# Performance work log

Measured on AMD Instinct MI355X. Metric: run time of the kernel, lower is better.

Reference implementation:

```python
import jax, jax.numpy as jnp
import numpy as np
from jax import lax

# Module constants (from init_kwargs)
B, C = 2, 64            # batch, in_channel
H, W, D = 64, 64, 64    # size
GROUPS = 2


def setup_inputs() -> dict:
    key = jax.random.key(0)
    ks = jax.random.split(key, 4)
    x = jax.random.normal(ks[0], (B, H * W * D, C), dtype=jnp.float32)
    # TransverseConv: Conv3d(2, W*2, (H,3,3), pad (0,1,1)) -> weight (O,I,kD,kH,kW)
    w_t = jax.random.normal(ks[1], (W * GROUPS, GROUPS, H, 3, 3), dtype=jnp.float32) * 0.02
    b_t = jnp.zeros((W * GROUPS,), jnp.float32)
    # CoronalConv: Conv3d(2, W*2, (3,3,D), pad (1,1,0))
    w_c = jax.random.normal(ks[2], (W * GROUPS, GROUPS, 3, 3, D), dtype=jnp.float32) * 0.02
    b_c = jnp.zeros((W * GROUPS,), jnp.float32)
    # map: Conv3d(2C, C, 1) stored as dense (C, 2C)
    w_map = jax.random.normal(ks[3], (C, 2 * C), dtype=jnp.float32) * 0.02
    b_map = jnp.zeros((C,), jnp.float32)
    return {"x": x, "w_t": w_t, "b_t": b_t, "w_c": w_c, "b_c": b_c,
            "w_map": w_map, "b_map": b_map}


def _forward(x, w_t, b_t, w_c, b_c, w_map, b_map):
    Bx, N, Cx = x.shape
    xg = x.transpose(0, 2, 1).reshape(Bx, Cx, H, W, D)   # (B,C,H,W,D)
    shortcut = xg
    xr = xg.reshape(Bx * Cx // GROUPS, GROUPS, H, W, D)
    dn = ('NCDHW', 'OIDHW', 'NCDHW')
    # Transverse: kernel spans full H -> output (B*C/2, 2W, 1, W, D)
    tans = lax.conv_general_dilated(xr, w_t, (1, 1, 1), [(0, 0), (1, 1), (1, 1)],
                                    dimension_numbers=dn)
    tans = tans + b_t[None, :, None, None, None]
    tans = tans.reshape(Bx, Cx, W, W, D)                 # (B,C,W,W,D)
    # Coronal: kernel spans full D -> output (B*C/2, 2W, H, W, 1)
    cor = lax.conv_general_dilated(xr, w_c, (1, 1, 1), [(1, 1), (1, 1), (0, 0)],
                                   dimension_numbers=dn)
    cor = cor + b_c[None, :, None, None, None]
    cor = cor.reshape(Bx, Cx, W, H, W)                   # (B,C,W,H,W)
    t1 = tans.transpose(0, 1, 3, 2, 4)                   # (B,C,W,W,D)
    c1 = cor.transpose(0, 1, 4, 3, 2)                    # (B,C,W,H,W)
    f = jnp.matmul(c1, t1).transpose(0, 1, 3, 2, 4)      # (B,C,H,W,D)
    attn = jnp.matmul(cor, tans).transpose(0, 1, 3, 2, 4)  # (B,C,H,W,D)
    cat = jnp.concatenate([shortcut * f, attn], axis=1)  # (B,2C,H,W,D)
    mapped = jnp.einsum('bkhwd,ck->bchwd', cat, w_map) + b_map[None, :, None, None, None]
    out = jax.nn.gelu(mapped, approximate=False)         # torch nn.GELU = exact erf
    return out.reshape(Bx, Cx, -1).transpose(0, 2, 1)    # (B,N,C)


def reference(x, w_t, b_t, w_c, b_c, w_map, b_map):
    return _forward(x, w_t, b_t, w_c, b_c, w_map, b_map)
```

## Files before the change

kernel.cpp:

```cpp
#include <hip/hip_runtime.h>
#include <hip/hip_bf16.h>
#include <math.h>

#define HWD 262144

typedef __attribute__((ext_vector_type(8))) short bf16x8;
typedef __attribute__((ext_vector_type(16))) float f32x16;

__device__ inline unsigned short bfu(float f) {
    __hip_bfloat16 h = __float2bfloat16(f);
    return *reinterpret_cast<unsigned short*>(&h);
}

__global__ void k_prep(const float* __restrict__ w_t, const float* __restrict__ w_c,
                       const float* __restrict__ w_map,
                       __hip_bfloat16* __restrict__ A_t, __hip_bfloat16* __restrict__ A_c,
                       __hip_bfloat16* __restrict__ Wb) {
    int i = blockIdx.x * 256 + threadIdx.x;
    if (i < 147456) {
        int kk = i & 15, oc = (i >> 4) & 127, ks = i >> 11;
        int z4 = ks & 3, kq = ks >> 2;
        int g = kq / 9, tap = kq - 9 * g;
        int z = z4 * 16 + kk;
        A_t[i] = __float2bfloat16(w_t[((oc * 2 + g) * 64 + z) * 9 + tap]);
        A_c[i] = __float2bfloat16(w_c[((oc * 2 + g) * 9 + tap) * 64 + z]);
    }
    if (i < 8192) {
        Wb[i] = __float2bfloat16(w_map[i]);
    }
}

__device__ inline void pack_row_bf16(__hip_bfloat16* dst, const float* src) {
    unsigned short u[16];
#pragma unroll
    for (int j = 0; j < 16; ++j) u[j] = bfu(src[j]);
    uint4* q = reinterpret_cast<uint4*>(dst);
    q[0] = *reinterpret_cast<const uint4*>(&u[0]);
    q[1] = *reinterpret_cast<const uint4*>(&u[8]);
}

__global__ void k_trans_c(const float* __restrict__ x, __hip_bfloat16* __restrict__ Xc) {
    __shared__ unsigned short tile[256][68];
    int b = blockIdx.y;
    long n0 = (long)blockIdx.x * 256;
    int t = threadIdx.x;
    const float4* xp4 = (const float4*)(x + ((long)b * HWD + n0) * 64);
#pragma unroll
    for (int i = 0; i < 16; ++i) {
        int f4i = i * 256 + t;
        float4 v = xp4[f4i];
        int nl = f4i >> 4, c4 = (f4i & 15) * 4;
        ushort4 u;
        u.x = bfu(v.x); u.y = bfu(v.y); u.z = bfu(v.z); u.w = bfu(v.w);
        *(ushort4*)&tile[nl][c4] = u;
    }
    __syncthreads();
    int c = t >> 2, hwl = t & 3;
    int hw0 = blockIdx.x * 4;
    __hip_bfloat16* dst0 = Xc + (long)(b * 64 + c) * HWD + (long)(hw0 + hwl) * 16;
#pragma unroll
    for (int z4 = 0; z4 < 4; ++z4) {
        unsigned short u[16];
#pragma unroll
        for (int j = 0; j < 16; ++j) u[j] = tile[hwl * 64 + z4 * 16 + j][c];
        __hip_bfloat16* dst = dst0 + z4 * 65536;
        *(uint4*)dst = *(const uint4*)&u[0];
        *(uint4*)(dst + 8) = *(const uint4*)&u[8];
    }
}

__global__ void k_trans_t(const float* __restrict__ x, __hip_bfloat16* __restrict__ Xt) {
    __shared__ unsigned short tile[256][68];
    int b = blockIdx.y;
    int wd0 = blockIdx.x * 4;
    int t = threadIdx.x;
    const float* xb = x + (long)b * HWD * 64 + (long)wd0 * 64;
#pragma unroll
    for (int i = 0; i < 16; ++i) {
        int idx = i * 256 + t;
        int h = idx >> 6, f = idx & 63;
        float4 v = *(const float4*)(xb + (long)h * 262144 + f * 4);
        int wdl = f >> 4, c4 = (f & 15) * 4;
        ushort4 u;
        u.x = bfu(v.x); u.y = bfu(v.y); u.z = bfu(v.z); u.w = bfu(v.w);
        *(ushort4*)&tile[wdl * 64 + h][c4] = u;
    }
    __syncthreads();
    int c = t >> 2, wdl = t & 3;
    __hip_bfloat16* dst0 = Xt + (long)(b * 64 + c) * HWD + (long)(wd0 + wdl) * 16;
#pragma unroll
    for (int z4 = 0; z4 < 4; ++z4) {
        unsigned short u[16];
#pragma unroll
        for (int j = 0; j < 16; ++j) u[j] = tile[wdl * 64 + z4 * 16 + j][c];
        __hip_bfloat16* dst = dst0 + z4 * 65536;
        *(uint4*)dst = *(const uint4*)&u[0];
        *(uint4*)(dst + 8) = *(const uint4*)&u[8];
    }
}

__global__ __launch_bounds__(256, 3) void k_conv_mfma(
        const __hip_bfloat16* __restrict__ Xt, const __hip_bfloat16* __restrict__ At_,
        const float* __restrict__ bt, float* __restrict__ OutT,
        const __hip_bfloat16* __restrict__ Xc, const __hip_bfloat16* __restrict__ Ac_,
        const float* __restrict__ bcb, float* __restrict__ OutC) {
    int Lfull = blockIdx.x;
    int halfk = Lfull >> 11;
    int L = Lfull & 2047;
    const __hip_bfloat16* X = halfk ? Xc : Xt;
    const __hip_bfloat16* Aglob = halfk ? Ac_ : At_;
    const float* bias = halfk ? bcb : bt;
    float* Out = halfk ? OutC : OutT;

    int grp = (L & 7) * 8 + ((L >> 3) >> 5);
    int pt = (L >> 3) & 31;
    int b = grp >> 5, ch = grp & 31;
    int p0 = pt * 2;
    const short* Xg = (const short*)(X + ((long)(b * 64 + 2 * ch)) * HWD);
    const short* Ag = (const short*)Aglob;
    int t = threadIdx.x;
    int lane = t & 63, wv = t >> 6;
    int O0 = (wv >> 1) * 64;
    int N0 = (wv & 1) * 64;
    int lrow = lane & 31, lq = lane >> 5;

    __shared__ __align__(16) short Bsm[2][4][2][1024];

    f32x16 acc00 = {0}, acc01 = {0}, acc10 = {0}, acc11 = {0};

    int srow = t >> 1, shalf = t & 1;
    int spr = srow >> 6, sq = srow & 63;
    const uint4 zero4 = {0u, 0u, 0u, 0u};
    uint4 ld0, ld1, ld2, ld3;

    auto stage_load = [&](int kq) {
        int g = (kq >= 9) ? 1 : 0;
        int tap = kq - 9 * g;
        int r = tap / 3, s = tap - 3 * r;
        int pp = p0 + spr + r - 1, qq = sq + s - 1;
        bool ok = ((unsigned)pp < 64u) && ((unsigned)qq < 64u);
        const short* px = Xg + (long)g * HWD + (pp * 64 + qq) * 16 + shalf * 8;
        ld0 = ok ? *(const uint4*)(px)           : zero4;
        ld1 = ok ? *(const uint4*)(px + 65536)   : zero4;
        ld2 = ok ? *(const uint4*)(px + 131072)  : zero4;
        ld3 = ok ? *(const uint4*)(px + 196608)  : zero4;
    };
    auto stage_write = [&](int buf) {
        *(uint4*)&Bsm[buf][0][shalf][srow * 8] = ld0;
        *(uint4*)&Bsm[buf][1][shalf][srow * 8] = ld1;
        *(uint4*)&Bsm[buf][2][shalf][srow * 8] = ld2;
        *(uint4*)&Bsm[buf][3][shalf][srow * 8] = ld3;
    };

    stage_load(0);
    stage_write(0);
    __syncthreads();

    int buf = 0;
    for (int kq = 0; kq < 18; ++kq) {
        if (kq < 17) stage_load(kq + 1);
#pragma unroll
        for (int z4 = 0; z4 < 4; ++z4) {
            int ks = kq * 4 + z4;
            const short* Apk = Ag + ks * 2048 + (O0 + lrow) * 16 + lq * 8;
            uint4 a0u = *(const uint4*)(Apk);
            uint4 a1u = *(const uint4*)(Apk + 512);
            bf16x8 a0 = *(bf16x8*)&a0u;
            bf16x8 a1 = *(bf16x8*)&a1u;
            bf16x8 b0 = *(const bf16x8*)&Bsm[buf][z4][lq][(N0 + lrow) * 8];
            bf16x8 b1 = *(const bf16x8*)&Bsm[buf][z4][lq][(N0 + 32 + lrow) * 8];
            acc00 = __builtin_amdgcn_mfma_f32_32x32x16_bf16(a0, b0, acc00, 0, 0, 0);
            acc01 = __builtin_amdgcn_mfma_f32_32x32x16_bf16(a0, b1, acc01, 0, 0, 0);
            acc10 = __builtin_amdgcn_mfma_f32_32x32x16_bf16(a1, b0, acc10, 0, 0, 0);
            acc11 = __builtin_amdgcn_mfma_f32_32x32x16_bf16(a1, b1, acc11, 0, 0, 0);
        }
        if (kq < 17) {
            stage_write(buf ^ 1);
            __syncthreads();
            buf ^= 1;
        }
    }

    long base0 = ((long)(b * 64 + 2 * ch)) * HWD + (long)p0 * 64;
    int n0l = N0 + lrow, n1l = N0 + 32 + lrow;
    long noff0 = (long)(n0l >> 6) * 64 + (n0l & 63);
    long noff1 = (long)(n1l >> 6) * 64 + (n1l & 63);
#pragma unroll
    for (int reg = 0; reg < 16; ++reg) {
        int row = (reg & 3) + 8 * (reg >> 2) + 4 * lq;
        int oc0 = O0 + row, oc1 = O0 + 32 + row;
        long cb0 = base0 + (long)(oc0 >> 6) * HWD + (long)(oc0 & 63) * 4096;
        long cb1 = base0 + (long)(oc1 >> 6) * HWD + (long)(oc1 & 63) * 4096;
        float bs0 = bias[oc0], bs1 = bias[oc1];
        Out[cb0 + noff0] = acc00[reg] + bs0;
        Out[cb0 + noff1] = acc01[reg] + bs0;
        Out[cb1 + noff0] = acc10[reg] + bs1;
        Out[cb1 + noff1] = acc11[reg] + bs1;
    }
}

__global__ __launch_bounds__(256) void k_attn(const float* __restrict__ Cc,
        const float* __restrict__ T, __hip_bfloat16* __restrict__ At) {
    __shared__ __align__(16) __hip_bfloat16 Ms[64][72];
    __shared__ __align__(16) __hip_bfloat16 Ns[64][72];
    int L = blockIdx.x;
    int xcd = L & 7, j = L >> 3;
    int bc = xcd * 16 + (j >> 6), w2 = j & 63;
    const float* Ap = Cc + ((long)bc * 64 + w2) * 4096;
    const float* Bp = T + ((long)bc * 64 + w2) * 4096;
    int t = threadIdx.x;
#pragma unroll
    for (int i = 0; i < 4; ++i) {
        int f = i * 256 + t;
        int r = f >> 4, q4 = (f & 15) * 4;
        float4 v = *(const float4*)(Ap + r * 64 + q4);
        ushort4 u;
        u.x = bfu(v.x); u.y = bfu(v.y); u.z = bfu(v.z); u.w = bfu(v.w);
        *(ushort4*)&Ms[r][q4] = u;
        float4 w = *(const float4*)(Bp + r * 64 + q4);
        Ns[q4 + 0][r] = __float2bfloat16(w.x);
        Ns[q4 + 1][r] = __float2bfloat16(w.y);
        Ns[q4 + 2][r] = __float2bfloat16(w.z);
        Ns[q4 + 3][r] = __float2bfloat16(w.w);
    }
    __syncthreads();
    int lane = t & 63, wv = t >> 6;
    int lrow = lane & 31, lhalf = lane >> 5;
    int hq = wv >> 1, dq = wv & 1;
    f32x16 acc = {0};
#pragma unroll
    for (int ks = 0; ks < 4; ++ks) {
        bf16x8 a = *(const bf16x8*)&Ms[hq * 32 + lrow][ks * 16 + lhalf * 8];
        bf16x8 bfr = *(const bf16x8*)&Ns[dq * 32 + lrow][ks * 16 + lhalf * 8];
        acc = __builtin_amdgcn_mfma_f32_32x32x16_bf16(a, bfr, acc, 0, 0, 0);
    }
    __hip_bfloat16* Ao = At + (long)bc * HWD + w2 * 64 + dq * 32 + lrow;
#pragma unroll
    for (int reg = 0; reg < 16; ++reg) {
        int hh = hq * 32 + (reg & 3) + 8 * (reg >> 2) + 4 * lhalf;
        Ao[(long)hh * 4096] = __float2bfloat16(acc[reg]);
    }
}

__global__ __launch_bounds__(512, 4) void k_f(const float* __restrict__ Cc,
        const float* __restrict__ T, __hip_bfloat16* __restrict__ F) {
    __shared__ __align__(16) __hip_bfloat16 As[8][64][24];
    __shared__ __align__(16) __hip_bfloat16 Ns[8][64][24];
    int L = blockIdx.x;
    int xcd = L & 7, j = L >> 3;
    int bc = xcd * 16 + (j >> 3), wt = j & 7;
    const float* Ab = Cc + (long)bc * HWD;
    const float* Bb = T + (long)bc * HWD;
    int t = threadIdx.x;
    int lane = t & 63, wv = t >> 6;
    int lrow = lane & 31, lhalf = lane >> 5;
    f32x16 acc00 = {0}, acc01 = {0}, acc10 = {0}, acc11 = {0};

    for (int w2c = 0; w2c < 4; ++w2c) {
        __syncthreads();
#pragma unroll
        for (int i = 0; i < 4; ++i) {
            int f = i * 512 + t;
            int half = f & 1, hh = (f >> 1) & 63, kk = f >> 7;
            float4 v = *(const float4*)(Ab + (long)(w2c * 16 + kk) * 4096 + hh * 64 + wt * 8 + half * 4);
            As[half * 4 + 0][hh][kk] = __float2bfloat16(v.x);
            As[half * 4 + 1][hh][kk] = __float2bfloat16(v.y);
            As[half * 4 + 2][hh][kk] = __float2bfloat16(v.z);
            As[half * 4 + 3][hh][kk] = __float2bfloat16(v.w);
        }
#pragma unroll
        for (int i = 0; i < 4; ++i) {
            int f = i * 512 + t;
            int d4 = f & 15, ww = (f >> 4) & 7, kk = f >> 7;
            float4 v = *(const float4*)(Bb + (long)(w2c * 16 + kk) * 4096 + (wt * 8 + ww) * 64 + d4 * 4);
            Ns[ww][d4 * 4 + 0][kk] = __float2bfloat16(v.x);
            Ns[ww][d4 * 4 + 1][kk] = __float2bfloat16(v.y);
            Ns[ww][d4 * 4 + 2][kk] = __float2bfloat16(v.z);
            Ns[ww][d4 * 4 + 3][kk] = __float2bfloat16(v.w);
        }
        __syncthreads();
        bf16x8 a0 = *(const bf16x8*)&As[wv][lrow][lhalf * 8];
        bf16x8 a1 = *(const bf16x8*)&As[wv][32 + lrow][lhalf * 8];
        bf16x8 b0 = *(const bf16x8*)&Ns[wv][lrow][lhalf * 8];
        bf16x8 b1 = *(const bf16x8*)&Ns[wv][32 + lrow][lhalf * 8];
        acc00 = __builtin_amdgcn_mfma_f32_32x32x16_bf16(a0, b0, acc00, 0, 0, 0);
        acc01 = __builtin_amdgcn_mfma_f32_32x32x16_bf16(a0, b1, acc01, 0, 0, 0);
        acc10 = __builtin_amdgcn_mfma_f32_32x32x16_bf16(a1, b0, acc10, 0, 0, 0);
        acc11 = __builtin_amdgcn_mfma_f32_32x32x16_bf16(a1, b1, acc11, 0, 0, 0);
    }
    __hip_bfloat16* Fp = F + (long)bc * HWD + (wt * 8 + wv) * 64;
#pragma unroll
    for (int reg = 0; reg < 16; ++reg) {
        int row = (reg & 3) + 8 * (reg >> 2) + 4 * lhalf;
        Fp[(long)row * 4096 + lrow]             = __float2bfloat16(acc00[reg]);
        Fp[(long)row * 4096 + 32 + lrow]        = __float2bfloat16(acc01[reg]);
        Fp[(long)(32 + row) * 4096 + lrow]      = __float2bfloat16(acc10[reg]);
        Fp[(long)(32 + row) * 4096 + 32 + lrow] = __float2bfloat16(acc11[reg]);
    }
}

__global__ __launch_bounds__(256, 3) void k_map(const float* __restrict__ x,
        const __hip_bfloat16* __restrict__ F, const __hip_bfloat16* __restrict__ At,
        const __hip_bfloat16* __restrict__ Wb, const float* __restrict__ b_map,
        float* __restrict__ out) {
    __shared__ float xs[2][16][257];
    __shared__ __hip_bfloat16 fa[2][16][264];

    int t = threadIdx.x;
    long n0 = (long)blockIdx.x * 256;
    int b = (int)(n0 >> 18);
    long nn0 = n0 & (HWD - 1);
    const float* xblk = x + n0 * 64;
    const __hip_bfloat16* Fb = F + (long)b * 64 * HWD + nn0;
    const __hip_bfloat16* Ab = At + (long)b * 64 * HWD + nn0;

    int lane = t & 63, wv = t >> 6;
    int lrow = lane & 31, lhalf = lane >> 5;

    const short* Wp = (const short*)Wb;
    bf16x8 wb0[8], wb1[8];
#pragma unroll
    for (int kc = 0; kc < 8; ++kc) {
        uint4 u0 = *(const uint4*)(Wp + lrow * 128 + kc * 16 + lhalf * 8);
        uint4 u1 = *(const uint4*)(Wp + (32 + lrow) * 128 + kc * 16 + lhalf * 8);
        wb0[kc] = *(bf16x8*)&u0;
        wb1[kc] = *(bf16x8*)&u1;
    }

    f32x16 acc00 = {0}, acc01 = {0}, acc10 = {0}, acc11 = {0};

    float4 xa, xb_, xc_, xd;
    uint4 fe, ff;
    int nrA = t >> 2, j4A = (t & 3) * 4;
    int rowF0 = t >> 5, segF0 = t & 31;
    int rowF1 = (256 + t) >> 5, segF1 = t & 31;

    auto load_chunk = [&](int kc) {
        if (kc < 4) {
            xa  = *(const float4*)(xblk + (nrA +   0) * 64 + kc * 16 + j4A);
            xb_ = *(const float4*)(xblk + (nrA +  64) * 64 + kc * 16 + j4A);
            xc_ = *(const float4*)(xblk + (nrA + 128) * 64 + kc * 16 + j4A);
            xd  = *(const float4*)(xblk + (nrA + 192) * 64 + kc * 16 + j4A);
            fe = *(const uint4*)(Fb + (long)(kc * 16 + rowF0) * HWD + segF0 * 8);
            ff = *(const uint4*)(Fb + (long)(kc * 16 + rowF1) * HWD + segF1 * 8);
        } else {
            fe = *(const uint4*)(Ab + (long)((kc - 4) * 16 + rowF0) * HWD + segF0 * 8);
            ff = *(const uint4*)(Ab + (long)((kc - 4) * 16 + rowF1) * HWD + segF1 * 8);
        }
    };
    auto write_chunk = [&](int kc, int buf) {
        if (kc < 4) {
            xs[buf][j4A + 0][nrA +   0] = xa.x;
            xs[buf][j4A + 1][nrA +   0] = xa.y;
            xs[buf][j4A + 2][nrA +   0] = xa.z;
            xs[buf][j4A + 3][nrA +   0] = xa.w;
            xs[buf][j4A + 0][nrA +  64] = xb_.x;
            xs[buf][j4A + 1][nrA +  64] = xb_.y;
            xs[buf][j4A + 2][nrA +  64] = xb_.z;
            xs[buf][j4A + 3][nrA +  64] = xb_.w;
            xs[buf][j4A + 0][nrA + 128] = xc_.x;
            xs[buf][j4A + 1][nrA + 128] = xc_.y;
            xs[buf][j4A + 2][nrA + 128] = xc_.z;
            xs[buf][j4A + 3][nrA + 128] = xc_.w;
            xs[buf][j4A + 0][nrA + 192] = xd.x;
            xs[buf][j4A + 1][nrA + 192] = xd.y;
            xs[buf][j4A + 2][nrA + 192] = xd.z;
            xs[buf][j4A + 3][nrA + 192] = xd.w;
        }
        *(uint4*)&fa[buf][rowF0][segF0 * 8] = fe;
        *(uint4*)&fa[buf][rowF1][segF1 * 8] = ff;
    };

    load_chunk(0);
    write_chunk(0, 0);
    __syncthreads();

#pragma unroll
    for (int kc = 0; kc < 8; ++kc) {
        int buf = kc & 1;
        if (kc < 7) load_chunk(kc + 1);
        unsigned short pv[16];
        if (kc < 4) {
#pragma unroll
            for (int k2 = 0; k2 < 16; ++k2) {
                float p = xs[buf][k2][t] * __bfloat162float(fa[buf][k2][t]);
                pv[k2] = bfu(p);
            }
        } else {
#pragma unroll
            for (int k2 = 0; k2 < 16; ++k2)
                pv[k2] = *reinterpret_cast<const unsigned short*>(&fa[buf][k2][t]);
        }
        unsigned lo0 = (unsigned)pv[0]  | ((unsigned)pv[1]  << 16);
        unsigned lo1 = (unsigned)pv[2]  | ((unsigned)pv[3]  << 16);
        unsigned lo2 = (unsigned)pv[4]  | ((unsigned)pv[5]  << 16);
        unsigned lo3 = (unsigned)pv[6]  | ((unsigned)pv[7]  << 16);
        unsigned hi0 = (unsigned)pv[8]  | ((unsigned)pv[9]  << 16);
        unsigned hi1 = (unsigned)pv[10] | ((unsigned)pv[11] << 16);
        unsigned hi2 = (unsigned)pv[12] | ((unsigned)pv[13] << 16);
        unsigned hi3 = (unsigned)pv[14] | ((unsigned)pv[15] << 16);
        int sl0 = lane & 31, sl1 = lane | 32;
        bool lowh = lane < 32;
        unsigned s00 = __shfl(hi0, sl0), s01 = __shfl(hi1, sl0);
        unsigned s02 = __shfl(hi2, sl0), s03 = __shfl(hi3, sl0);
        unsigned r00 = __shfl(lo0, sl1), r01 = __shfl(lo1, sl1);
        unsigned r02 = __shfl(lo2, sl1), r03 = __shfl(lo3, sl1);
        uint4 ua0, ua1;
        ua0.x = lowh ? lo0 : s00; ua0.y = lowh ? lo1 : s01;
        ua0.z = lowh ? lo2 : s02; ua0.w = lowh ? lo3 : s03;
        ua1.x = lowh ? r00 : hi0; ua1.y = lowh ? r01 : hi1;
        ua1.z = lowh ? r02 : hi2; ua1.w = lowh ? r03 : hi3;
        bf16x8 a0 = *(bf16x8*)&ua0;
        bf16x8 a1 = *(bf16x8*)&ua1;
        acc00 = __builtin_amdgcn_mfma_f32_32x32x16_bf16(a0, wb0[kc], acc00, 0, 0, 0);
        acc01 = __builtin_amdgcn_mfma_f32_32x32x16_bf16(a0, wb1[kc], acc01, 0, 0, 0);
        acc10 = __builtin_amdgcn_mfma_f32_32x32x16_bf16(a1, wb0[kc], acc10, 0, 0, 0);
        acc11 = __builtin_amdgcn_mfma_f32_32x32x16_bf16(a1, wb1[kc], acc11, 0, 0, 0);
        if (kc < 7) {
            write_chunk(kc + 1, buf ^ 1);
            __syncthreads();
        }
    }

    float bs0 = b_map[lrow];
    float bs1 = b_map[32 + lrow];
    const float inv_sqrt2 = 0.70710678118654752440f;
    float* ob = out + (n0 + wv * 64) * 64;
#pragma unroll
    for (int reg = 0; reg < 16; ++reg) {
        int nrow = (reg & 3) + 8 * (reg >> 2) + 4 * lhalf;
        float v00 = acc00[reg] + bs0;
        float v01 = acc01[reg] + bs1;
        float v10 = acc10[reg] + bs0;
        float v11 = acc11[reg] + bs1;
        v00 = 0.5f * v00 * (1.f + erff(v00 * inv_sqrt2));
        v01 = 0.5f * v01 * (1.f + erff(v01 * inv_sqrt2));
        v10 = 0.5f * v10 * (1.f + erff(v10 * inv_sqrt2));
        v11 = 0.5f * v11 * (1.f + erff(v11 * inv_sqrt2));
        ob[(long)nrow * 64 + lrow] = v00;
        ob[(long)nrow * 64 + 32 + lrow] = v01;
        ob[(long)(32 + nrow) * 64 + lrow] = v10;
        ob[(long)(32 + nrow) * 64 + 32 + lrow] = v11;
    }
}

extern "C" void kernel_launch(void* const* d_in, const int* in_sizes, int n_in,
                              void* d_out, int out_size, void* d_ws, size_t ws_size,
                              hipStream_t stream) {
    const float* x     = (const float*)d_in[0];
    const float* w_t   = (const float*)d_in[1];
    const float* b_t   = (const float*)d_in[2];
    const float* w_c   = (const float*)d_in[3];
    const float* b_c   = (const float*)d_in[4];
    const float* w_map = (const float*)d_in[5];
    const float* b_map = (const float*)d_in[6];
    float* out = (float*)d_out;
    float* ws = (float*)d_ws;

    __hip_bfloat16* Xc = (__hip_bfloat16*)ws;
    __hip_bfloat16* Xt = (__hip_bfloat16*)(ws + 16777216L);
    float* T = ws + 33554432L;
    float* Cc = out;
    __hip_bfloat16* A_t = (__hip_bfloat16*)(ws + 67108864L);
    __hip_bfloat16* A_c = (__hip_bfloat16*)(ws + 67182592L);
    __hip_bfloat16* Wb = (__hip_bfloat16*)(ws + 67256320L);
    __hip_bfloat16* At_bf = Xc;
    __hip_bfloat16* F_bf = Xt;

    hipLaunchKernelGGL(k_prep, dim3(576), dim3(256), 0, stream, w_t, w_c, w_map, A_t, A_c, Wb);
    hipLaunchKernelGGL(k_trans_c, dim3(1024, 2), dim3(256), 0, stream, x, Xc);
    hipLaunchKernelGGL(k_trans_t, dim3(1024, 2), dim3(256), 0, stream, x, Xt);
    hipLaunchKernelGGL(k_conv_mfma, dim3(4096), dim3(256), 0, stream,
                       Xt, A_t, b_t, T, Xc, A_c, b_c, Cc);
    hipLaunchKernelGGL(k_attn, dim3(8192), dim3(256), 0, stream, Cc, T, At_bf);
    hipLaunchKernelGGL(k_f, dim3(1024), dim3(512), 0, stream, Cc, T, F_bf);
    hipLaunchKernelGGL(k_map, dim3(2048), dim3(256), 0, stream, x, F_bf, At_bf, Wb, b_map, out);
}
```

Before: 714.0 us.

## Double conv MFMA tile width to four rows per block for weight reuse

```diff
diff --git a/kernel.cpp b/kernel.cpp
--- a/kernel.cpp
+++ b/kernel.cpp
@@ -99,39 +99,40 @@
     }
 }
 
-__global__ __launch_bounds__(256, 3) void k_conv_mfma(
+__global__ __launch_bounds__(256, 2) void k_conv_mfma(
         const __hip_bfloat16* __restrict__ Xt, const __hip_bfloat16* __restrict__ At_,
         const float* __restrict__ bt, float* __restrict__ OutT,
         const __hip_bfloat16* __restrict__ Xc, const __hip_bfloat16* __restrict__ Ac_,
         const float* __restrict__ bcb, float* __restrict__ OutC) {
     int Lfull = blockIdx.x;
-    int halfk = Lfull >> 11;
-    int L = Lfull & 2047;
+    int halfk = Lfull >> 10;
+    int L = Lfull & 1023;
     const __hip_bfloat16* X = halfk ? Xc : Xt;
     const __hip_bfloat16* Aglob = halfk ? Ac_ : At_;
     const float* bias = halfk ? bcb : bt;
     float* Out = halfk ? OutC : OutT;
 
-    int grp = (L & 7) * 8 + ((L >> 3) >> 5);
-    int pt = (L >> 3) & 31;
+    int xcd = L & 7, j = L >> 3;
+    int grp = xcd * 8 + (j >> 4);
+    int pt = j & 15;
     int b = grp >> 5, ch = grp & 31;
-    int p0 = pt * 2;
+    int p0 = pt * 4;
     const short* Xg = (const short*)(X + ((long)(b * 64 + 2 * ch)) * HWD);
     const short* Ag = (const short*)Aglob;
     int t = threadIdx.x;
     int lane = t & 63, wv = t >> 6;
     int O0 = (wv >> 1) * 64;
-    int N0 = (wv & 1) * 64;
+    int N0 = (wv & 1) * 128;
     int lrow = lane & 31, lq = lane >> 5;
 
-    __shared__ __align__(16) short Bsm[2][4][2][1024];
-
-    f32x16 acc00 = {0}, acc01 = {0}, acc10 = {0}, acc11 = {0};
-
-    int srow = t >> 1, shalf = t & 1;
-    int spr = srow >> 6, sq = srow & 63;
+    __shared__ __align__(16) short Bsm[2][4][2][2048];
+
+    f32x16 a00 = {0}, a01 = {0}, a02 = {0}, a03 = {0};
+    f32x16 a10 = {0}, a11 = {0}, a12 = {0}, a13 = {0};
+
+    int spr = t >> 6, sq = t & 63;
     const uint4 zero4 = {0u, 0u, 0u, 0u};
-    uint4 ld0, ld1, ld2, ld3;
+    uint4 l00, l01, l10, l11, l20, l21, l30, l31;
 
     auto stage_load = [&](int kq) {
         int g = (kq >= 9) ? 1 : 0;
@@ -139,17 +140,25 @@
         int r = tap / 3, s = tap - 3 * r;
         int pp = p0 + spr + r - 1, qq = sq + s - 1;
         bool ok = ((unsigned)pp < 64u) && ((unsigned)qq < 64u);
-        const short* px = Xg + (long)g * HWD + (pp * 64 + qq) * 16 + shalf * 8;
-        ld0 = ok ? *(const uint4*)(px)           : zero4;
-        ld1 = ok ? *(const uint4*)(px + 65536)   : zero4;
-        ld2 = ok ? *(const uint4*)(px + 131072)  : zero4;
-        ld3 = ok ? *(const uint4*)(px + 196608)  : zero4;
+        const short* px = Xg + (long)g * HWD + (pp * 64 + qq) * 16;
+        l00 = ok ? *(const uint4*)(px)               : zero4;
+        l01 = ok ? *(const uint4*)(px + 8)           : zero4;
+        l10 = ok ? *(const uint4*)(px + 65536)       : zero4;
+        l11 = ok ? *(const uint4*)(px + 65536 + 8)   : zero4;
+        l20 = ok ? *(const uint4*)(px + 131072)      : zero4;
+        l21 = ok ? *(const uint4*)(px + 131072 + 8)  : zero4;
+        l30 = ok ? *(const uint4*)(px + 196608)      : zero4;
+        l31 = ok ? *(const uint4*)(px + 196608 + 8)  : zero4;
     };
     auto stage_write = [&](int buf) {
-        *(uint4*)&Bsm[buf][0][shalf][srow * 8] = ld0;
-        *(uint4*)&Bsm[buf][1][shalf][srow * 8] = ld1;
-        *(uint4*)&Bsm[buf][2][shalf][srow * 8] = ld2;
-        *(uint4*)&Bsm[buf][3][shalf][srow * 8] = ld3;
+        *(uint4*)&Bsm[buf][0][0][t * 8] = l00;
+        *(uint4*)&Bsm[buf][0][1][t * 8] = l01;
+        *(uint4*)&Bsm[buf][1][0][t * 8] = l10;
+        *(uint4*)&Bsm[buf][1][1][t * 8] = l11;
+        *(uint4*)&Bsm[buf][2][0][t * 8] = l20;
+        *(uint4*)&Bsm[buf][2][1][t * 8] = l21;
+        *(uint4*)&Bsm[buf][3][0][t * 8] = l30;
+        *(uint4*)&Bsm[buf][3][1][t * 8] = l31;
     };
 
     stage_load(0);
@@ -165,14 +174,20 @@
             const short* Apk = Ag + ks * 2048 + (O0 + lrow) * 16 + lq * 8;
             uint4 a0u = *(const uint4*)(Apk);
             uint4 a1u = *(const uint4*)(Apk + 512);
-            bf16x8 a0 = *(bf16x8*)&a0u;
-            bf16x8 a1 = *(bf16x8*)&a1u;
+            bf16x8 fa0 = *(bf16x8*)&a0u;
+            bf16x8 fa1 = *(bf16x8*)&a1u;
             bf16x8 b0 = *(const bf16x8*)&Bsm[buf][z4][lq][(N0 + lrow) * 8];
             bf16x8 b1 = *(const bf16x8*)&Bsm[buf][z4][lq][(N0 + 32 + lrow) * 8];
-            acc00 = __builtin_amdgcn_mfma_f32_32x32x16_bf16(a0, b0, acc00, 0, 0, 0);
-            acc01 = __builtin_amdgcn_mfma_f32_32x32x16_bf16(a0, b1, acc01, 0, 0, 0);
-            acc10 = __builtin_amdgcn_mfma_f32_32x32x16_bf16(a1, b0, acc10, 0, 0, 0);
-            acc11 = __builtin_amdgcn_mfma_f32_32x32x16_bf16(a1, b1, acc11, 0, 0, 0);
+            bf16x8 b2 = *(const bf16x8*)&Bsm[buf][z4][lq][(N0 + 64 + lrow) * 8];
+            bf16x8 b3 = *(const bf16x8*)&Bsm[buf][z4][lq][(N0 + 96 + lrow) * 8];
+            a00 = __builtin_amdgcn_mfma_f32_32x32x16_bf16(fa0, b0, a00, 0, 0, 0);
+            a01 = __builtin_amdgcn_mfma_f32_32x32x16_bf16(fa0, b1, a01, 0, 0, 0);
+            a02 = __builtin_amdgcn_mfma_f32_32x32x16_bf16(fa0, b2, a02, 0, 0, 0);
+            a03 = __builtin_amdgcn_mfma_f32_32x32x16_bf16(fa0, b3, a03, 0, 0, 0);
+            a10 = __builtin_amdgcn_mfma_f32_32x32x16_bf16(fa1, b0, a10, 0, 0, 0);
+            a11 = __builtin_amdgcn_mfma_f32_32x32x16_bf16(fa1, b1, a11, 0, 0, 0);
+            a12 = __builtin_amdgcn_mfma_f32_32x32x16_bf16(fa1, b2, a12, 0, 0, 0);
+            a13 = __builtin_amdgcn_mfma_f32_32x32x16_bf16(fa1, b3, a13, 0, 0, 0);
         }
         if (kq < 17) {
             stage_write(buf ^ 1);
@@ -182,9 +197,6 @@
     }
 
     long base0 = ((long)(b * 64 + 2 * ch)) * HWD + (long)p0 * 64;
-    int n0l = N0 + lrow, n1l = N0 + 32 + lrow;
-    long noff0 = (long)(n0l >> 6) * 64 + (n0l & 63);
-    long noff1 = (long)(n1l >> 6) * 64 + (n1l & 63);
 #pragma unroll
     for (int reg = 0; reg < 16; ++reg) {
         int row = (reg & 3) + 8 * (reg >> 2) + 4 * lq;
@@ -192,10 +204,14 @@
         long cb0 = base0 + (long)(oc0 >> 6) * HWD + (long)(oc0 & 63) * 4096;
         long cb1 = base0 + (long)(oc1 >> 6) * HWD + (long)(oc1 & 63) * 4096;
         float bs0 = bias[oc0], bs1 = bias[oc1];
-        Out[cb0 + noff0] = acc00[reg] + bs0;
-        Out[cb0 + noff1] = acc01[reg] + bs0;
-        Out[cb1 + noff0] = acc10[reg] + bs1;
-        Out[cb1 + noff1] = acc11[reg] + bs1;
+        Out[cb0 + N0 + lrow]      = a00[reg] + bs0;
+        Out[cb0 + N0 + 32 + lrow] = a01[reg] + bs0;
+        Out[cb0 + N0 + 64 + lrow] = a02[reg] + bs0;
+        Out[cb0 + N0 + 96 + lrow] = a03[reg] + bs0;
+        Out[cb1 + N0 + lrow]      = a10[reg] + bs1;
+        Out[cb1 + N0 + 32 + lrow] = a11[reg] + bs1;
+        Out[cb1 + N0 + 64 + lrow] = a12[reg] + bs1;
+        Out[cb1 + N0 + 96 + lrow] = a13[reg] + bs1;
     }
 }
 
@@ -470,7 +486,7 @@
     hipLaunchKernelGGL(k_prep, dim3(576), dim3(256), 0, stream, w_t, w_c, w_map, A_t, A_c, Wb);
     hipLaunchKernelGGL(k_trans_c, dim3(1024, 2), dim3(256), 0, stream, x, Xc);
     hipLaunchKernelGGL(k_trans_t, dim3(1024, 2), dim3(256), 0, stream, x, Xt);
-    hipLaunchKernelGGL(k_conv_mfma, dim3(4096), dim3(256), 0, stream,
+    hipLaunchKernelGGL(k_conv_mfma, dim3(2048), dim3(256), 0, stream,
                        Xt, A_t, b_t, T, Xc, A_c, b_c, Cc);
     hipLaunchKernelGGL(k_attn, dim3(8192), dim3(256), 0, stream, Cc, T, At_bf);
     hipLaunchKernelGGL(k_f, dim3(1024), dim3(512), 0, stream, Cc, T, F_bf);
```

Measured after the change: 727.8 us. Within noise of the previous version (+1.9%).
